# Optimization experiments

Measured on AMD Instinct MI355X. Metric: run time of the kernel, lower is better.

## Reference

```python
import jax, jax.numpy as jnp
import numpy as np

B = 64            # number of graphs
NPG = 64          # nodes per graph (static; lengths are all equal here)
N = B * NPG       # total nodes = sum(lengths)
LT = 128          # max text tokens per node
LL = 32           # max labels per node
VOCAB = 50000
TOTAL_NUM = 100000
D = 256           # embedding_text == embedding_label == hidden_dimension
OUT = 1024


def setup_inputs() -> dict:
    key = jax.random.key(0)
    ks = jax.random.split(key, 12)
    return {
        "text_ids": jax.random.randint(ks[0], (N, LT), 0, VOCAB),
        "label_ids": jax.random.randint(ks[1], (N, LL), 0, TOTAL_NUM),
        "text_len": jax.random.randint(ks[2], (N,), 1, LT + 1),
        "label_len": jax.random.randint(ks[3], (N,), 1, LL + 1),
        "word_emb": jax.random.normal(ks[4], (VOCAB, D), jnp.float32) * 0.02,
        "label_emb": jax.random.normal(ks[5], (TOTAL_NUM, D), jnp.float32) * 0.02,
        "Wg_text": jax.random.normal(ks[6], (D, D), jnp.float32) * (1.0 / np.sqrt(D)),
        "Wg_label": jax.random.normal(ks[7], (D, D), jnp.float32) * (1.0 / np.sqrt(D)),
        "w_adap": jax.random.normal(ks[8], (2,), jnp.float32),
        "W1": jax.random.normal(ks[9], (D, D), jnp.float32) * (1.0 / np.sqrt(D)),
        "b1": jnp.zeros((D,), jnp.float32),
        "Wout": jax.random.normal(ks[10], (D, OUT), jnp.float32) * (1.0 / np.sqrt(D)),
        "bout": jnp.zeros((OUT,), jnp.float32),
    }


def _ragged_bag(table, ids, lens, mean):
    # gather rows then masked sum over the ragged axis (EmbeddingBag-style)
    L = ids.shape[1]
    mask = (jnp.arange(L)[None, :] < lens[:, None]).astype(table.dtype)  # [N, L]
    emb = table[ids]                                                     # [N, L, D]
    out = jnp.einsum("nld,nl->nd", emb, mask)
    if mean:
        out = out / lens[:, None].astype(table.dtype)
    return out


def reference(text_ids, label_ids, text_len, label_len, word_emb, label_emb,
              Wg_text, Wg_label, w_adap, W1, b1, Wout, bout):
    # fetchFeature: per-node ragged mean of word embeddings, ragged sum of label embeddings
    text_out = _ragged_bag(word_emb, text_ids, text_len, mean=True)    # [N, D]
    label_out = _ragged_bag(label_emb, label_ids, label_len, mean=False)  # [N, D]

    # weighted_GCN surrogate: per-type linear projection + relu, then per-graph mean readout
    h_t = jax.nn.relu(text_out @ Wg_text)   # [N, D]
    h_l = jax.nn.relu(label_out @ Wg_label)  # [N, D]
    seg = jnp.repeat(jnp.arange(B), NPG)     # graph id per node
    r_t = jax.ops.segment_sum(h_t, seg, num_segments=B) / NPG  # [B, D]
    r_l = jax.ops.segment_sum(h_l, seg, num_segments=B) / NPG  # [B, D]

    # adap: Linear(2,1,bias=False) over stacked (text,label), then MLLinear fusion
    fused = jnp.stack([r_t, r_l], axis=-1) @ w_adap  # [B, D]
    h = jax.nn.relu(fused @ W1 + b1)
    return h @ Wout + bout  # [B, OUT]
```

## Files before the change

kernel.cpp:

```cpp
#include <hip/hip_runtime.h>

#define NN      4096
#define BG      64
#define NPG_    64
#define LT_     128
#define LL_     32
#define D_      256
#define OUT_    1024
#define NPBF    4

__global__ __launch_bounds__(256, 4) void fused_kernel(
    const int*   __restrict__ text_ids,
    const int*   __restrict__ label_ids,
    const int*   __restrict__ text_len,
    const int*   __restrict__ label_len,
    const float* __restrict__ word_emb,
    const float* __restrict__ label_emb,
    const float* __restrict__ Wg_text,
    const float* __restrict__ Wg_label,
    const float* __restrict__ w_adap,
    float*       __restrict__ h_comb)
{
    __shared__ int   sIds[NPBF][LT_ + LL_];
    __shared__ float red[4][NPBF * D_];
    __shared__ float xT[NPBF][D_ + 8];
    __shared__ float xL[NPBF][D_ + 8];

    const int tid  = threadIdx.x;
    const int wave = tid >> 6;
    const int lane = tid & 63;
    const int base = blockIdx.x * NPBF;

    for (int idx = tid; idx < NPBF * LT_; idx += 256) {
        const int nd = idx >> 7, t = idx & (LT_ - 1);
        sIds[nd][t] = text_ids[(size_t)(base + nd) * LT_ + t];
    }
    if (tid < NPBF * LL_) {
        const int nd = tid >> 5, t = tid & (LL_ - 1);
        sIds[nd][LT_ + t] = label_ids[(size_t)(base + nd) * LL_ + t];
    }
    int lt[NPBF], ll[NPBF];
    #pragma unroll
    for (int nd = 0; nd < NPBF; ++nd) {
        lt[nd] = text_len[base + nd];
        ll[nd] = label_len[base + nd];
    }
    __syncthreads();

    float4 aT[NPBF], aL[NPBF];
    {
        const float* __restrict__ bp = word_emb + (size_t)lane * 4;
        #pragma unroll
        for (int nd = 0; nd < NPBF; ++nd) {
            float4 a = make_float4(0.f, 0.f, 0.f, 0.f);
            #pragma unroll 8
            for (int l = wave; l < lt[nd]; l += 4) {
                const float4 v = *reinterpret_cast<const float4*>(
                    bp + (size_t)sIds[nd][l] * D_);
                a.x += v.x; a.y += v.y; a.z += v.z; a.w += v.w;
            }
            aT[nd] = a;
        }
    }
    {
        const float* __restrict__ bp = label_emb + (size_t)lane * 4;
        #pragma unroll
        for (int nd = 0; nd < NPBF; ++nd) {
            float4 a = make_float4(0.f, 0.f, 0.f, 0.f);
            #pragma unroll 8
            for (int l = wave; l < ll[nd]; l += 4) {
                const float4 v = *reinterpret_cast<const float4*>(
                    bp + (size_t)sIds[nd][LT_ + l] * D_);
                a.x += v.x; a.y += v.y; a.z += v.z; a.w += v.w;
            }
            aL[nd] = a;
        }
    }

    #pragma unroll
    for (int nd = 0; nd < NPBF; ++nd)
        *reinterpret_cast<float4*>(&red[wave][nd * D_ + lane * 4]) = aT[nd];
    __syncthreads();
    #pragma unroll
    for (int i = 0; i < NPBF; ++i) {
        const int idx = tid + 256 * i;
        const float v = (red[0][idx] + red[1][idx]) + (red[2][idx] + red[3][idx]);
        xT[i][tid] = v / (float)lt[i];
    }
    __syncthreads();
    #pragma unroll
    for (int nd = 0; nd < NPBF; ++nd)
        *reinterpret_cast<float4*>(&red[wave][nd * D_ + lane * 4]) = aL[nd];
    __syncthreads();
    #pragma unroll
    for (int i = 0; i < NPBF; ++i) {
        const int idx = tid + 256 * i;
        xL[i][tid] = (red[0][idx] + red[1][idx]) + (red[2][idx] + red[3][idx]);
    }
    __syncthreads();

    float pT[NPBF][4], pL[NPBF][4];
    #pragma unroll
    for (int nd = 0; nd < NPBF; ++nd) {
        #pragma unroll
        for (int j = 0; j < 4; ++j) { pT[nd][j] = 0.f; pL[nd][j] = 0.f; }
    }
    const int c0 = lane * 4;
    const int k0 = wave * 64;

    for (int k4 = 0; k4 < 64; k4 += 4) {
        const int k = k0 + k4;
        float xt[NPBF][4], xl[NPBF][4];
        #pragma unroll
        for (int nd = 0; nd < NPBF; ++nd) {
            const float4 a = *reinterpret_cast<const float4*>(&xT[nd][k]);
            const float4 b = *reinterpret_cast<const float4*>(&xL[nd][k]);
            xt[nd][0] = a.x; xt[nd][1] = a.y; xt[nd][2] = a.z; xt[nd][3] = a.w;
            xl[nd][0] = b.x; xl[nd][1] = b.y; xl[nd][2] = b.z; xl[nd][3] = b.w;
        }
        #pragma unroll
        for (int dk = 0; dk < 4; ++dk) {
            const size_t ro = (size_t)(k + dk) * D_ + c0;
            const float4 wt = *reinterpret_cast<const float4*>(Wg_text  + ro);
            const float4 wl = *reinterpret_cast<const float4*>(Wg_label + ro);
            #pragma unroll
            for (int nd = 0; nd < NPBF; ++nd) {
                const float xv = xt[nd][dk];
                pT[nd][0] = fmaf(xv, wt.x, pT[nd][0]);
                pT[nd][1] = fmaf(xv, wt.y, pT[nd][1]);
                pT[nd][2] = fmaf(xv, wt.z, pT[nd][2]);
                pT[nd][3] = fmaf(xv, wt.w, pT[nd][3]);
                const float yv = xl[nd][dk];
                pL[nd][0] = fmaf(yv, wl.x, pL[nd][0]);
                pL[nd][1] = fmaf(yv, wl.y, pL[nd][1]);
                pL[nd][2] = fmaf(yv, wl.z, pL[nd][2]);
                pL[nd][3] = fmaf(yv, wl.w, pL[nd][3]);
            }
        }
    }

    #pragma unroll
    for (int nd = 0; nd < NPBF; ++nd)
        *reinterpret_cast<float4*>(&red[wave][nd * D_ + c0]) =
            make_float4(pT[nd][0], pT[nd][1], pT[nd][2], pT[nd][3]);
    __syncthreads();
    float rT[NPBF];
    #pragma unroll
    for (int i = 0; i < NPBF; ++i) {
        const int idx = tid + 256 * i;
        rT[i] = (red[0][idx] + red[1][idx]) + (red[2][idx] + red[3][idx]);
    }
    __syncthreads();
    #pragma unroll
    for (int nd = 0; nd < NPBF; ++nd)
        *reinterpret_cast<float4*>(&red[wave][nd * D_ + c0]) =
            make_float4(pL[nd][0], pL[nd][1], pL[nd][2], pL[nd][3]);
    __syncthreads();

    const float w0 = w_adap[0] * (1.0f / (float)NPG_);
    const float w1 = w_adap[1] * (1.0f / (float)NPG_);
    #pragma unroll
    for (int i = 0; i < NPBF; ++i) {
        const int idx = tid + 256 * i;
        const float rL = (red[0][idx] + red[1][idx]) + (red[2][idx] + red[3][idx]);
        const float ht = rT[i] > 0.f ? rT[i] : 0.f;
        const float hl = rL    > 0.f ? rL    : 0.f;
        h_comb[(size_t)(base + i) * D_ + tid] = w0 * ht + w1 * hl;
    }
}

__global__ __launch_bounds__(256) void graph_kernel(
    const float* __restrict__ h_comb,
    const float* __restrict__ W1,
    const float* __restrict__ b1,
    const float* __restrict__ Wout,
    const float* __restrict__ bout,
    float*       __restrict__ out)
{
    __shared__ float fused[D_];
    __shared__ float hrow[D_];

    const int bx   = blockIdx.x;
    const int b    = bx >> 2;
    const int part = bx & 3;
    const int tid  = threadIdx.x;

    float acc = 0.f;
    const float* __restrict__ basep = h_comb + (size_t)b * NPG_ * D_ + tid;
    #pragma unroll 8
    for (int n = 0; n < NPG_; ++n) acc += basep[(size_t)n * D_];
    fused[tid] = acc;
    __syncthreads();

    float a1 = b1[tid];
    for (int d = 0; d < D_; ++d)
        a1 = fmaf(fused[d], W1[(size_t)d * D_ + tid], a1);
    hrow[tid] = a1 > 0.f ? a1 : 0.f;
    __syncthreads();

    const int j = part * 256 + tid;
    float o = bout[j];
    for (int d = 0; d < D_; ++d)
        o = fmaf(hrow[d], Wout[(size_t)d * OUT_ + j], o);
    out[(size_t)b * OUT_ + j] = o;
}

extern "C" void kernel_launch(void* const* d_in, const int* in_sizes, int n_in,
                              void* d_out, int out_size, void* d_ws, size_t ws_size,
                              hipStream_t stream) {
    const int*   text_ids  = (const int*)  d_in[0];
    const int*   label_ids = (const int*)  d_in[1];
    const int*   text_len  = (const int*)  d_in[2];
    const int*   label_len = (const int*)  d_in[3];
    const float* word_emb  = (const float*)d_in[4];
    const float* label_emb = (const float*)d_in[5];
    const float* Wg_text   = (const float*)d_in[6];
    const float* Wg_label  = (const float*)d_in[7];
    const float* w_adap    = (const float*)d_in[8];
    const float* W1        = (const float*)d_in[9];
    const float* b1        = (const float*)d_in[10];
    const float* Wout      = (const float*)d_in[11];
    const float* bout      = (const float*)d_in[12];

    float* h_comb = (float*)d_ws;
    float* out    = (float*)d_out;

    fused_kernel<<<NN / NPBF, 256, 0, stream>>>(
        text_ids, label_ids, text_len, label_len,
        word_emb, label_emb, Wg_text, Wg_label, w_adap, h_comb);

    graph_kernel<<<BG * 4, 256, 0, stream>>>(
        h_comb, W1, b1, Wout, bout, out);
}
```

Baseline: 89.75 us.

## Process eight nodes per 512-thread block to halve projection weight reads

Each block now handles eight nodes with eight waves instead of four nodes with four. Gather loops stride over eight waves, and the cross-wave reduction folds the upper four waves into a four-slot shared buffer before the final sum. The projection matmul splits K over eight waves, so each Wg row load is reused across eight nodes, halving global weight traffic per node. In exchange each block uses more registers and shared memory, has more barriers, and there are half as many blocks, which may hurt occupancy and latency hiding for the gather.

```diff
diff --git a/kernel.cpp b/kernel.cpp
--- a/kernel.cpp
+++ b/kernel.cpp
@@ -7,9 +7,10 @@
 #define LL_     32
 #define D_      256
 #define OUT_    1024
-#define NPBF    4
-
-__global__ __launch_bounds__(256, 4) void fused_kernel(
+#define NPB8    8
+#define BLK     512
+
+__global__ __launch_bounds__(BLK, 4) void fused_kernel(
     const int*   __restrict__ text_ids,
     const int*   __restrict__ label_ids,
     const int*   __restrict__ text_len,
@@ -21,40 +22,45 @@
     const float* __restrict__ w_adap,
     float*       __restrict__ h_comb)
 {
-    __shared__ int   sIds[NPBF][LT_ + LL_];
-    __shared__ float red[4][NPBF * D_];
-    __shared__ float xT[NPBF][D_ + 8];
-    __shared__ float xL[NPBF][D_ + 8];
+    __shared__ int   sIds[NPB8][LT_ + LL_];
+    __shared__ float red4[4][NPB8 * D_];
+    __shared__ float xT[NPB8][D_ + 8];
+    __shared__ float xL[NPB8][D_ + 8];
+    __shared__ int   sLT[NPB8], sLL[NPB8];
+    __shared__ float sInvT[NPB8];
 
     const int tid  = threadIdx.x;
     const int wave = tid >> 6;
     const int lane = tid & 63;
-    const int base = blockIdx.x * NPBF;
-
-    for (int idx = tid; idx < NPBF * LT_; idx += 256) {
+    const int base = blockIdx.x * NPB8;
+
+    #pragma unroll
+    for (int r = 0; r < 2; ++r) {
+        const int idx = tid + BLK * r;
         const int nd = idx >> 7, t = idx & (LT_ - 1);
         sIds[nd][t] = text_ids[(size_t)(base + nd) * LT_ + t];
     }
-    if (tid < NPBF * LL_) {
+    if (tid < NPB8 * LL_) {
         const int nd = tid >> 5, t = tid & (LL_ - 1);
         sIds[nd][LT_ + t] = label_ids[(size_t)(base + nd) * LL_ + t];
     }
-    int lt[NPBF], ll[NPBF];
-    #pragma unroll
-    for (int nd = 0; nd < NPBF; ++nd) {
-        lt[nd] = text_len[base + nd];
-        ll[nd] = label_len[base + nd];
-    }
-    __syncthreads();
-
-    float4 aT[NPBF], aL[NPBF];
+    if (tid < NPB8) {
+        const int l = text_len[base + tid];
+        sLT[tid] = l;
+        sInvT[tid] = 1.0f / (float)l;
+        sLL[tid] = label_len[base + tid];
+    }
+    __syncthreads();
+
+    float4 aT[NPB8], aL[NPB8];
     {
         const float* __restrict__ bp = word_emb + (size_t)lane * 4;
         #pragma unroll
-        for (int nd = 0; nd < NPBF; ++nd) {
+        for (int nd = 0; nd < NPB8; ++nd) {
+            const int L = sLT[nd];
             float4 a = make_float4(0.f, 0.f, 0.f, 0.f);
-            #pragma unroll 8
-            for (int l = wave; l < lt[nd]; l += 4) {
+            #pragma unroll 4
+            for (int l = wave; l < L; l += 8) {
                 const float4 v = *reinterpret_cast<const float4*>(
                     bp + (size_t)sIds[nd][l] * D_);
                 a.x += v.x; a.y += v.y; a.z += v.z; a.w += v.w;
@@ -65,10 +71,11 @@
     {
         const float* __restrict__ bp = label_emb + (size_t)lane * 4;
         #pragma unroll
-        for (int nd = 0; nd < NPBF; ++nd) {
+        for (int nd = 0; nd < NPB8; ++nd) {
+            const int L = sLL[nd];
             float4 a = make_float4(0.f, 0.f, 0.f, 0.f);
-            #pragma unroll 8
-            for (int l = wave; l < ll[nd]; l += 4) {
+            #pragma unroll 2
+            for (int l = wave; l < L; l += 8) {
                 const float4 v = *reinterpret_cast<const float4*>(
                     bp + (size_t)sIds[nd][LT_ + l] * D_);
                 a.x += v.x; a.y += v.y; a.z += v.z; a.w += v.w;
@@ -77,42 +84,68 @@
         }
     }
 
-    #pragma unroll
-    for (int nd = 0; nd < NPBF; ++nd)
-        *reinterpret_cast<float4*>(&red[wave][nd * D_ + lane * 4]) = aT[nd];
-    __syncthreads();
-    #pragma unroll
-    for (int i = 0; i < NPBF; ++i) {
-        const int idx = tid + 256 * i;
-        const float v = (red[0][idx] + red[1][idx]) + (red[2][idx] + red[3][idx]);
-        xT[i][tid] = v / (float)lt[i];
-    }
-    __syncthreads();
-    #pragma unroll
-    for (int nd = 0; nd < NPBF; ++nd)
-        *reinterpret_cast<float4*>(&red[wave][nd * D_ + lane * 4]) = aL[nd];
-    __syncthreads();
-    #pragma unroll
-    for (int i = 0; i < NPBF; ++i) {
-        const int idx = tid + 256 * i;
-        xL[i][tid] = (red[0][idx] + red[1][idx]) + (red[2][idx] + red[3][idx]);
-    }
-    __syncthreads();
-
-    float pT[NPBF][4], pL[NPBF][4];
-    #pragma unroll
-    for (int nd = 0; nd < NPBF; ++nd) {
+    if (wave < 4) {
+        #pragma unroll
+        for (int nd = 0; nd < NPB8; ++nd)
+            *reinterpret_cast<float4*>(&red4[wave][nd * D_ + lane * 4]) = aT[nd];
+    }
+    __syncthreads();
+    if (wave >= 4) {
+        #pragma unroll
+        for (int nd = 0; nd < NPB8; ++nd) {
+            float4* p = reinterpret_cast<float4*>(&red4[wave - 4][nd * D_ + lane * 4]);
+            float4 v = *p;
+            v.x += aT[nd].x; v.y += aT[nd].y; v.z += aT[nd].z; v.w += aT[nd].w;
+            *p = v;
+        }
+    }
+    __syncthreads();
+    #pragma unroll
+    for (int i = 0; i < 4; ++i) {
+        const int idx = tid + BLK * i;
+        const int nd = idx >> 8, col = idx & 255;
+        const float v = (red4[0][idx] + red4[1][idx]) + (red4[2][idx] + red4[3][idx]);
+        xT[nd][col] = v * sInvT[nd];
+    }
+    __syncthreads();
+    if (wave < 4) {
+        #pragma unroll
+        for (int nd = 0; nd < NPB8; ++nd)
+            *reinterpret_cast<float4*>(&red4[wave][nd * D_ + lane * 4]) = aL[nd];
+    }
+    __syncthreads();
+    if (wave >= 4) {
+        #pragma unroll
+        for (int nd = 0; nd < NPB8; ++nd) {
+            float4* p = reinterpret_cast<float4*>(&red4[wave - 4][nd * D_ + lane * 4]);
+            float4 v = *p;
+            v.x += aL[nd].x; v.y += aL[nd].y; v.z += aL[nd].z; v.w += aL[nd].w;
+            *p = v;
+        }
+    }
+    __syncthreads();
+    #pragma unroll
+    for (int i = 0; i < 4; ++i) {
+        const int idx = tid + BLK * i;
+        const int nd = idx >> 8, col = idx & 255;
+        xL[nd][col] = (red4[0][idx] + red4[1][idx]) + (red4[2][idx] + red4[3][idx]);
+    }
+    __syncthreads();
+
+    float pT[NPB8][4], pL[NPB8][4];
+    #pragma unroll
+    for (int nd = 0; nd < NPB8; ++nd) {
         #pragma unroll
         for (int j = 0; j < 4; ++j) { pT[nd][j] = 0.f; pL[nd][j] = 0.f; }
     }
     const int c0 = lane * 4;
-    const int k0 = wave * 64;
-
-    for (int k4 = 0; k4 < 64; k4 += 4) {
-        const int k = k0 + k4;
-        float xt[NPBF][4], xl[NPBF][4];
-        #pragma unroll
-        for (int nd = 0; nd < NPBF; ++nd) {
+    const int k0 = wave * 32;
+
+    for (int kk = 0; kk < 32; kk += 4) {
+        const int k = k0 + kk;
+        float xt[NPB8][4], xl[NPB8][4];
+        #pragma unroll
+        for (int nd = 0; nd < NPB8; ++nd) {
             const float4 a = *reinterpret_cast<const float4*>(&xT[nd][k]);
             const float4 b = *reinterpret_cast<const float4*>(&xL[nd][k]);
             xt[nd][0] = a.x; xt[nd][1] = a.y; xt[nd][2] = a.z; xt[nd][3] = a.w;
@@ -124,7 +157,7 @@
             const float4 wt = *reinterpret_cast<const float4*>(Wg_text  + ro);
             const float4 wl = *reinterpret_cast<const float4*>(Wg_label + ro);
             #pragma unroll
-            for (int nd = 0; nd < NPBF; ++nd) {
+            for (int nd = 0; nd < NPB8; ++nd) {
                 const float xv = xt[nd][dk];
                 pT[nd][0] = fmaf(xv, wt.x, pT[nd][0]);
                 pT[nd][1] = fmaf(xv, wt.y, pT[nd][1]);
@@ -139,33 +172,58 @@
         }
     }
 
-    #pragma unroll
-    for (int nd = 0; nd < NPBF; ++nd)
-        *reinterpret_cast<float4*>(&red[wave][nd * D_ + c0]) =
-            make_float4(pT[nd][0], pT[nd][1], pT[nd][2], pT[nd][3]);
-    __syncthreads();
-    float rT[NPBF];
-    #pragma unroll
-    for (int i = 0; i < NPBF; ++i) {
-        const int idx = tid + 256 * i;
-        rT[i] = (red[0][idx] + red[1][idx]) + (red[2][idx] + red[3][idx]);
-    }
-    __syncthreads();
-    #pragma unroll
-    for (int nd = 0; nd < NPBF; ++nd)
-        *reinterpret_cast<float4*>(&red[wave][nd * D_ + c0]) =
-            make_float4(pL[nd][0], pL[nd][1], pL[nd][2], pL[nd][3]);
+    if (wave < 4) {
+        #pragma unroll
+        for (int nd = 0; nd < NPB8; ++nd)
+            *reinterpret_cast<float4*>(&red4[wave][nd * D_ + c0]) =
+                make_float4(pT[nd][0], pT[nd][1], pT[nd][2], pT[nd][3]);
+    }
+    __syncthreads();
+    if (wave >= 4) {
+        #pragma unroll
+        for (int nd = 0; nd < NPB8; ++nd) {
+            float4* p = reinterpret_cast<float4*>(&red4[wave - 4][nd * D_ + c0]);
+            float4 v = *p;
+            v.x += pT[nd][0]; v.y += pT[nd][1]; v.z += pT[nd][2]; v.w += pT[nd][3];
+            *p = v;
+        }
+    }
+    __syncthreads();
+    float rT[4];
+    #pragma unroll
+    for (int i = 0; i < 4; ++i) {
+        const int idx = tid + BLK * i;
+        rT[i] = (red4[0][idx] + red4[1][idx]) + (red4[2][idx] + red4[3][idx]);
+    }
+    __syncthreads();
+    if (wave < 4) {
+        #pragma unroll
+        for (int nd = 0; nd < NPB8; ++nd)
+            *reinterpret_cast<float4*>(&red4[wave][nd * D_ + c0]) =
+                make_float4(pL[nd][0], pL[nd][1], pL[nd][2], pL[nd][3]);
+    }
+    __syncthreads();
+    if (wave >= 4) {
+        #pragma unroll
+        for (int nd = 0; nd < NPB8; ++nd) {
+            float4* p = reinterpret_cast<float4*>(&red4[wave - 4][nd * D_ + c0]);
+            float4 v = *p;
+            v.x += pL[nd][0]; v.y += pL[nd][1]; v.z += pL[nd][2]; v.w += pL[nd][3];
+            *p = v;
+        }
+    }
     __syncthreads();
 
     const float w0 = w_adap[0] * (1.0f / (float)NPG_);
     const float w1 = w_adap[1] * (1.0f / (float)NPG_);
     #pragma unroll
-    for (int i = 0; i < NPBF; ++i) {
-        const int idx = tid + 256 * i;
-        const float rL = (red[0][idx] + red[1][idx]) + (red[2][idx] + red[3][idx]);
+    for (int i = 0; i < 4; ++i) {
+        const int idx = tid + BLK * i;
+        const int nd = idx >> 8, col = idx & 255;
+        const float rL = (red4[0][idx] + red4[1][idx]) + (red4[2][idx] + red4[3][idx]);
         const float ht = rT[i] > 0.f ? rT[i] : 0.f;
         const float hl = rL    > 0.f ? rL    : 0.f;
-        h_comb[(size_t)(base + i) * D_ + tid] = w0 * ht + w1 * hl;
+        h_comb[(size_t)(base + nd) * D_ + col] = w0 * ht + w1 * hl;
     }
 }
 
@@ -225,7 +283,7 @@
     float* h_comb = (float*)d_ws;
     float* out    = (float*)d_out;
 
-    fused_kernel<<<NN / NPBF, 256, 0, stream>>>(
+    fused_kernel<<<NN / NPB8, BLK, 0, stream>>>(
         text_ids, label_ids, text_len, label_len,
         word_emb, label_emb, Wg_text, Wg_label, w_adap, h_comb);
 
```

New measurement: 148.1 us. 1.65x slower.
